# Optimization experiments

Measured on AMD Instinct MI355X. Metric: run time of the kernel, lower is better.

The kernel has to match this reference:

```python
import jax, jax.numpy as jnp
import numpy as np

NUM_EMBEDDINGS = 1024
EMBEDDING_DIM = 256
COMMITMENT_COST = 0.25


def setup_inputs() -> dict:
    key = jax.random.key(0)
    k1, k2 = jax.random.split(key)
    inputs = jax.random.normal(k1, (16, EMBEDDING_DIM, 4096), dtype=jnp.float32)
    # torch init: uniform(-1/K, 1/K)
    weight = jax.random.uniform(k2, (NUM_EMBEDDINGS, EMBEDDING_DIM), dtype=jnp.float32,
                                minval=-1.0 / NUM_EMBEDDINGS, maxval=1.0 / NUM_EMBEDDINGS)
    return {"inputs": inputs, "weight": weight}


def reference(inputs, weight):
    # [B, D, T] -> [B, T, D]
    x = jnp.transpose(inputs, (0, 2, 1))
    B, T, D = x.shape
    x_flat = x.reshape(-1, D)  # [N, D]
    distances = (jnp.sum(x_flat ** 2, axis=1, keepdims=True)
                 + jnp.sum(weight ** 2, axis=1)
                 - 2.0 * jnp.matmul(x_flat, weight.T))  # [N, K]
    encoding_indices = jnp.argmin(distances, axis=1)  # [N]
    # gather instead of one-hot matmul (same math)
    quantized = weight[encoding_indices].reshape(B, T, D)

    e_latent_loss = jnp.mean((jax.lax.stop_gradient(quantized) - x) ** 2)
    q_latent_loss = jnp.mean((quantized - jax.lax.stop_gradient(x)) ** 2)
    loss = q_latent_loss + COMMITMENT_COST * e_latent_loss

    # straight-through estimator
    quantized_st = x + jax.lax.stop_gradient(quantized - x)

    N = x_flat.shape[0]
    counts = jnp.zeros((weight.shape[0],), dtype=jnp.float32).at[encoding_indices].add(1.0)
    avg_probs = counts / N
    perplexity = jnp.exp(-jnp.sum(avg_probs * jnp.log(avg_probs + 1e-10)))

    return quantized_st, loss, perplexity, encoding_indices[:, None]
```

## Files before the change

### kernel.cpp

```cpp
#include <hip/hip_runtime.h>
#include <math.h>

#define B_ 16
#define D_ 256
#define T_ 4096
#define K_ 1024
#define N_ (B_*T_)

typedef __attribute__((ext_vector_type(8))) short short8;
typedef __attribute__((ext_vector_type(8))) unsigned short ushort8;
typedef __attribute__((ext_vector_type(4))) float f32x4;

#define CAND_MAX 24
#define EPS1 1.0e-3f
#define EPS2 5.0e-4f

__device__ __forceinline__ unsigned short f2bf(float f) {
  unsigned u = __float_as_uint(f);
  u += 0x7fffu + ((u >> 16) & 1u);
  return (unsigned short)(u >> 16);
}

__device__ __forceinline__ void gl_lds16(const void* g, void* l) {
  __builtin_amdgcn_global_load_lds((const __attribute__((address_space(1))) unsigned int*)g,
                                   (__attribute__((address_space(3))) unsigned int*)l,
                                   16, 0, 0);
}

__global__ void k_split(const float* __restrict__ x, unsigned short* __restrict__ xh) {
  __shared__ float xs[64 * 65];
  const int b = blockIdx.y, t0 = blockIdx.x * 64;
  const int tid = threadIdx.x;
  const int r = tid >> 4, cf = tid & 15;
  for (int dc = 0; dc < D_; dc += 64) {
#pragma unroll
    for (int p = 0; p < 4; ++p) {
      const int dd = r + p * 16;
      float4 v = *(const float4*)(x + (size_t)b * D_ * T_ + (size_t)(dc + dd) * T_ + t0 + cf * 4);
      xs[(cf * 4 + 0) * 65 + dd] = v.x;
      xs[(cf * 4 + 1) * 65 + dd] = v.y;
      xs[(cf * 4 + 2) * 65 + dd] = v.z;
      xs[(cf * 4 + 3) * 65 + dd] = v.w;
    }
    __syncthreads();
    const int c = tid & 7, row2 = tid >> 3;
#pragma unroll
    for (int p = 0; p < 2; ++p) {
      const int tt = row2 + p * 32;
      ushort8 hv;
#pragma unroll
      for (int j = 0; j < 8; ++j) hv[j] = f2bf(xs[tt * 65 + c * 8 + j]);
      *(ushort8*)(xh + (size_t)(b * T_ + t0 + tt) * D_ + dc + c * 8) = hv;
    }
    __syncthreads();
  }
}

__global__ void k_wsplit(const float* __restrict__ w, unsigned short* __restrict__ wh) {
  const int i = blockIdx.x * 256 + threadIdx.x;
  if (i < K_ * D_) wh[i] = f2bf(w[i]);
}

__global__ void k_wsq(const float* __restrict__ w, float* __restrict__ wsq) {
#pragma clang fp contract(off)
  const int k = blockIdx.x * 256 + threadIdx.x;
  const float* row = w + (size_t)k * D_;
  float h[2];
#pragma unroll
  for (int half = 0; half < 2; ++half) {
    const float* a = row + half * 128;
    float r[8];
#pragma unroll
    for (int j = 0; j < 8; ++j) { float v = a[j]; r[j] = v * v; }
    for (int i = 8; i < 128; i += 8) {
#pragma unroll
      for (int j = 0; j < 8; ++j) { float v = a[i + j]; r[j] += v * v; }
    }
    h[half] = ((r[0] + r[1]) + (r[2] + r[3])) + ((r[4] + r[5]) + (r[6] + r[7]));
  }
  wsq[k] = h[0] + h[1];
}

__global__ void k_xsq(const float* __restrict__ x, float* __restrict__ xsq) {
#pragma clang fp contract(off)
  const int t = blockIdx.x * 256 + threadIdx.x;
  const int b = blockIdx.y;
  const float* p = x + (size_t)b * D_ * T_ + t;
  float h[2];
#pragma unroll
  for (int half = 0; half < 2; ++half) {
    const float* ph = p + (size_t)half * 128 * T_;
    float r[8];
#pragma unroll
    for (int j = 0; j < 8; ++j) { float v = ph[(size_t)j * T_]; r[j] = v * v; }
    for (int i = 8; i < 128; i += 8) {
#pragma unroll
      for (int j = 0; j < 8; ++j) { float v = ph[(size_t)(i + j) * T_]; r[j] += v * v; }
    }
    h[half] = ((r[0] + r[1]) + (r[2] + r[3])) + ((r[4] + r[5]) + (r[6] + r[7]));
  }
  xsq[(size_t)b * T_ + t] = h[0] + h[1];
}

__launch_bounds__(256, 4)
__global__ void k_mfma(const unsigned short* __restrict__ xh, const unsigned short* __restrict__ wh,
                       const float* __restrict__ xsq, const float* __restrict__ wsq,
                       int* __restrict__ cnt, int2* __restrict__ cand) {
  __shared__ unsigned short Ah[128 * 32];
  __shared__ unsigned short Bh[128 * 32];
  const int tid = threadIdx.x;
  const int wave = tid >> 6, lane = tid & 63;
  const int col = lane & 15, quad = lane >> 4;
  const int n0 = blockIdx.x * 128;
  const int k0 = blockIdx.y * 128;
  const int wm = wave >> 1, wn = wave & 1;

  const int srow_base = (wave & 1) * 64;
  unsigned short* stile = (wave < 2) ? Ah : Bh;
  const unsigned short* sg = (wave < 2) ? (xh + (size_t)n0 * D_) : (wh + (size_t)k0 * D_);
  const int sq = (lane & 3) ^ ((lane >> 3) & 3);
  const int smrow = lane >> 2;

  int aoff[4], boff[4];
#pragma unroll
  for (int f = 0; f < 4; ++f) {
    const int mt = wm * 64 + f * 16 + col;
    aoff[f] = mt * 32 + (quad ^ ((col >> 1) & 3)) * 8;
    const int nt = wn * 64 + f * 16 + col;
    boff[f] = nt * 32 + (quad ^ ((col >> 1) & 3)) * 8;
  }

  f32x4 acc[4][4] = {};
  for (int dc = 0; dc < D_; dc += 32) {
#pragma unroll
    for (int i = 0; i < 4; ++i) {
      const int m = srow_base + i * 16 + smrow;
      gl_lds16(sg + (size_t)m * D_ + dc + sq * 8, &stile[(srow_base + i * 16) * 32]);
    }
    __syncthreads();
    short8 a[4], b[4];
#pragma unroll
    for (int f = 0; f < 4; ++f) a[f] = *(const short8*)(Ah + aoff[f]);
#pragma unroll
    for (int f = 0; f < 4; ++f) b[f] = *(const short8*)(Bh + boff[f]);
#pragma unroll
    for (int fm = 0; fm < 4; ++fm)
#pragma unroll
      for (int fn = 0; fn < 4; ++fn)
        acc[fm][fn] = __builtin_amdgcn_mfma_f32_16x16x32_bf16(a[fm], b[fn], acc[fm][fn], 0, 0, 0);
    __syncthreads();
  }

  float xq[4][4], wq[4];
#pragma unroll
  for (int fm = 0; fm < 4; ++fm)
#pragma unroll
    for (int r = 0; r < 4; ++r) xq[fm][r] = xsq[n0 + wm * 64 + fm * 16 + quad * 4 + r];
#pragma unroll
  for (int fn = 0; fn < 4; ++fn) wq[fn] = wsq[k0 + wn * 64 + fn * 16 + col];

  float rmin[4][4];
#pragma unroll
  for (int fm = 0; fm < 4; ++fm)
#pragma unroll
    for (int r = 0; r < 4; ++r) {
      float v = INFINITY;
#pragma unroll
      for (int fn = 0; fn < 4; ++fn) {
        const float s = (xq[fm][r] + wq[fn]) - 2.0f * acc[fm][fn][r];
        v = fminf(v, s);
      }
      v = fminf(v, __shfl_xor(v, 1));
      v = fminf(v, __shfl_xor(v, 2));
      v = fminf(v, __shfl_xor(v, 4));
      v = fminf(v, __shfl_xor(v, 8));
      rmin[fm][r] = v;
    }

  float* minbuf = (float*)Ah;
  if (col == 0) {
#pragma unroll
    for (int fm = 0; fm < 4; ++fm)
#pragma unroll
      for (int r = 0; r < 4; ++r)
        minbuf[(wm * 64 + fm * 16 + quad * 4 + r) * 2 + wn] = rmin[fm][r];
  }
  __syncthreads();

#pragma unroll
  for (int fm = 0; fm < 4; ++fm)
#pragma unroll
    for (int r = 0; r < 4; ++r) {
      const int m = wm * 64 + fm * 16 + quad * 4 + r;
      const float th = fminf(minbuf[2 * m], minbuf[2 * m + 1]) + EPS1;
#pragma unroll
      for (int fn = 0; fn < 4; ++fn) {
        const float s = (xq[fm][r] + wq[fn]) - 2.0f * acc[fm][fn][r];
        if (s <= th) {
          const int p = atomicAdd(&cnt[n0 + m], 1);
          if (p < CAND_MAX)
            cand[(size_t)(n0 + m) * CAND_MAX + p] =
                make_int2(k0 + wn * 64 + fn * 16 + col, __float_as_int(s));
        }
      }
    }
}

__global__ void k_rescore(const float* __restrict__ x, const float* __restrict__ w,
                          const float* __restrict__ xsq, const float* __restrict__ wsq,
                          const int* __restrict__ cnt, const int2* __restrict__ cand,
                          int* __restrict__ final_idx) {
  __shared__ float xrow[64 * 257];
  __shared__ unsigned int sbits[64];
  __shared__ unsigned long long fin[64];
  const int blk = blockIdx.x;
  const int b = (blk * 64) >> 12, t0 = (blk * 64) & (T_ - 1);
  const int tid = threadIdx.x;
  const int r = tid >> 4, cf = tid & 15;
  if (tid < 64) { sbits[tid] = 0xffffffffu; fin[tid] = ~0ULL; }
  for (int dc = 0; dc < D_; dc += 64) {
#pragma unroll
    for (int p = 0; p < 4; ++p) {
      const int dd = r + p * 16;
      float4 v = *(const float4*)(x + (size_t)b * D_ * T_ + (size_t)(dc + dd) * T_ + t0 + cf * 4);
      xrow[(cf * 4 + 0) * 257 + dc + dd] = v.x;
      xrow[(cf * 4 + 1) * 257 + dc + dd] = v.y;
      xrow[(cf * 4 + 2) * 257 + dc + dd] = v.z;
      xrow[(cf * 4 + 3) * 257 + dc + dd] = v.w;
    }
  }
  __syncthreads();
  const int row = tid & 63;
  const int n = blk * 64 + row;
  const int c0 = tid >> 6;
  const int nc = min(cnt[n], CAND_MAX);
  for (int c = c0; c < nc; c += 4)
    atomicMin(&sbits[row], (unsigned)cand[(size_t)n * CAND_MAX + c].y);
  __syncthreads();
  const float th = __uint_as_float(sbits[row]) + EPS2;
  const float xq = xsq[n];
  for (int c = c0; c < nc; c += 4) {
    const int2 e = cand[(size_t)n * CAND_MAX + c];
    if (__int_as_float(e.y) <= th) {
      const float* wr = w + (size_t)e.x * D_;
      float acc = 0.f;
#pragma unroll 8
      for (int d = 0; d < D_; ++d) acc = fmaf(xrow[row * 257 + d], wr[d], acc);
      const float s = (xq + wsq[e.x]) - 2.0f * acc;
      atomicMin(&fin[row], ((unsigned long long)__float_as_uint(s) << 32) | (unsigned)e.x);
    }
  }
  __syncthreads();
  if (tid < 64) final_idx[blk * 64 + tid] = (int)(fin[tid] & 0xffffffffULL);
}

__global__ void k_emit(const float* __restrict__ x, const float* __restrict__ w,
                       const int* __restrict__ fidx,
                       float* __restrict__ out0, float* __restrict__ out_idx,
                       int* __restrict__ counts, float* __restrict__ sumsq) {
  __shared__ float xs[64 * 65];
  __shared__ int sidx[64];
  __shared__ float sred[4];
  const int b = blockIdx.y, t0 = blockIdx.x * 64;
  const int tid = threadIdx.x;

  if (tid < 64) {
    const int n = b * T_ + t0 + tid;
    const int idx = fidx[n];
    sidx[tid] = idx;
    out_idx[n] = (float)idx;
    atomicAdd(&counts[idx], 1);
  }
  __syncthreads();

  const int r = tid >> 4;
  const int c = tid & 15;
  float lsum = 0.f;
  for (int dc = 0; dc < D_; dc += 64) {
#pragma unroll
    for (int p = 0; p < 4; ++p) {
      const int dd = r + p * 16;
      float4 v = *(const float4*)(x + (size_t)b * D_ * T_ + (size_t)(dc + dd) * T_ + t0 + c * 4);
      xs[(c * 4 + 0) * 65 + dd] = v.x;
      xs[(c * 4 + 1) * 65 + dd] = v.y;
      xs[(c * 4 + 2) * 65 + dd] = v.z;
      xs[(c * 4 + 3) * 65 + dd] = v.w;
    }
    __syncthreads();
    const int dx = tid & 15;
    const int tg = tid >> 4;
#pragma unroll
    for (int q = 0; q < 4; ++q) {
      const int t = q * 16 + tg;
      const int idx = sidx[t];
      const float4 wv = *(const float4*)(w + (size_t)idx * D_ + dc + dx * 4);
      const float x0 = xs[t * 65 + dx * 4 + 0];
      const float x1 = xs[t * 65 + dx * 4 + 1];
      const float x2 = xs[t * 65 + dx * 4 + 2];
      const float x3 = xs[t * 65 + dx * 4 + 3];
      const float d0 = wv.x - x0, d1 = wv.y - x1, d2 = wv.z - x2, d3 = wv.w - x3;
      float4 ov = make_float4(x0 + d0, x1 + d1, x2 + d2, x3 + d3);
      *(float4*)(out0 + (size_t)(b * T_ + t0 + t) * D_ + dc + dx * 4) = ov;
      lsum += d0 * d0 + d1 * d1 + d2 * d2 + d3 * d3;
    }
    __syncthreads();
  }
  for (int off = 32; off; off >>= 1) lsum += __shfl_down(lsum, off);
  if ((tid & 63) == 0) sred[tid >> 6] = lsum;
  __syncthreads();
  if (tid == 0) atomicAdd(sumsq, sred[0] + sred[1] + sred[2] + sred[3]);
}

__global__ void k_final(const int* __restrict__ counts, const float* __restrict__ sumsq,
                        float* __restrict__ out_scalars) {
  __shared__ float sred[4];
  const int tid = threadIdx.x;
  float s = 0.f;
  for (int k = tid; k < K_; k += 256) {
    const float p = (float)counts[k] / (float)N_;
    s += p * logf(p + 1e-10f);
  }
  for (int off = 32; off; off >>= 1) s += __shfl_down(s, off);
  if ((tid & 63) == 0) sred[tid >> 6] = s;
  __syncthreads();
  if (tid == 0) {
    const float ent = sred[0] + sred[1] + sred[2] + sred[3];
    const float m = sumsq[0] / 16777216.0f;
    out_scalars[0] = m + 0.25f * m;
    out_scalars[1] = expf(-ent);
  }
}

__global__ void k_wt(const float* __restrict__ w, float* __restrict__ wt) {
  __shared__ float tile[64][65];
  const int k0 = blockIdx.x * 64, d0 = blockIdx.y * 64;
  const int c = threadIdx.x & 15, r = threadIdx.x >> 4;
#pragma unroll
  for (int p = 0; p < 4; ++p) {
    const int kk = r + p * 16;
    float4 v = *(const float4*)(w + (size_t)(k0 + kk) * D_ + d0 + c * 4);
    tile[kk][c * 4 + 0] = v.x; tile[kk][c * 4 + 1] = v.y;
    tile[kk][c * 4 + 2] = v.z; tile[kk][c * 4 + 3] = v.w;
  }
  __syncthreads();
#pragma unroll
  for (int p = 0; p < 4; ++p) {
    const int dd = r + p * 16;
    float4 v = make_float4(tile[c * 4 + 0][dd], tile[c * 4 + 1][dd],
                           tile[c * 4 + 2][dd], tile[c * 4 + 3][dd]);
    *(float4*)(wt + (size_t)(d0 + dd) * K_ + k0 + c * 4) = v;
  }
}

__launch_bounds__(256, 4)
__global__ void k_argmin(const float* __restrict__ x, const float* __restrict__ wt,
                         const float* __restrict__ xsq, const float* __restrict__ wsq,
                         unsigned long long* __restrict__ packed) {
  extern __shared__ char smem[];
  float* Xs = (float*)smem;
  float* Ws = (float*)(smem + 32 * 128 * sizeof(float));
  const int tid = threadIdx.x;
  const int tx = tid & 15, ty = tid >> 4;
  const int n0 = blockIdx.x * 128, k0 = blockIdx.y * 128;
  const int b = n0 >> 12, t0 = n0 & (T_ - 1);
  const float* xbase = x + (size_t)b * D_ * T_ + t0;
  const float* wbase = wt + k0;
  float acc[8][8];
#pragma unroll
  for (int i = 0; i < 8; ++i)
#pragma unroll
    for (int j = 0; j < 8; ++j) acc[i][j] = 0.f;
  const int sr = tid >> 5, sc = tid & 31;
  for (int dc = 0; dc < D_; dc += 32) {
#pragma unroll
    for (int p = 0; p < 4; ++p) {
      const int rr = sr + p * 8;
      const float4 xv = *(const float4*)(xbase + (size_t)(dc + rr) * T_ + sc * 4);
      *(float4*)(Xs + rr * 128 + sc * 4) = xv;
      const float4 wv = *(const float4*)(wbase + (size_t)(dc + rr) * K_ + sc * 4);
      *(float4*)(Ws + rr * 128 + sc * 4) = wv;
    }
    __syncthreads();
#pragma unroll 4
    for (int d = 0; d < 32; ++d) {
      const float4 xa = *(const float4*)(Xs + d * 128 + tx * 8);
      const float4 xb = *(const float4*)(Xs + d * 128 + tx * 8 + 4);
      const float4 wa = *(const float4*)(Ws + d * 128 + ty * 8);
      const float4 wb = *(const float4*)(Ws + d * 128 + ty * 8 + 4);
      const float xr[8] = {xa.x, xa.y, xa.z, xa.w, xb.x, xb.y, xb.z, xb.w};
      const float wr[8] = {wa.x, wa.y, wa.z, wa.w, wb.x, wb.y, wb.z, wb.w};
#pragma unroll
      for (int i = 0; i < 8; ++i)
#pragma unroll
        for (int j = 0; j < 8; ++j)
          acc[i][j] = fmaf(xr[i], wr[j], acc[i][j]);
    }
    __syncthreads();
  }
  float xq[8];
#pragma unroll
  for (int i = 0; i < 8; ++i) xq[i] = xsq[n0 + tx * 8 + i];
  float best[8]; int bidx[8];
#pragma unroll
  for (int i = 0; i < 8; ++i) { best[i] = INFINITY; bidx[i] = 0; }
#pragma unroll
  for (int j = 0; j < 8; ++j) {
    const int kk = k0 + ty * 8 + j;
    const float wq = wsq[kk];
#pragma unroll
    for (int i = 0; i < 8; ++i) {
      const float s = (xq[i] + wq) - 2.0f * acc[i][j];
      if (s < best[i]) { best[i] = s; bidx[i] = kk; }
    }
  }
  float* rv = (float*)smem;
  int* ri = (int*)(smem + 16 * 128 * sizeof(float));
#pragma unroll
  for (int i = 0; i < 8; ++i) {
    rv[ty * 128 + tx * 8 + i] = best[i];
    ri[ty * 128 + tx * 8 + i] = bidx[i];
  }
  __syncthreads();
  if (tid < 128) {
    float bv = rv[tid]; int bi = ri[tid];
#pragma unroll
    for (int u = 1; u < 16; ++u) {
      const float v = rv[u * 128 + tid];
      const int ii = ri[u * 128 + tid];
      if (v < bv || (v == bv && ii < bi)) { bv = v; bi = ii; }
    }
    const unsigned long long pk =
        ((unsigned long long)__float_as_uint(bv) << 32) | (unsigned int)bi;
    atomicMin(packed + n0 + tid, pk);
  }
}

__global__ void k_unpack(const unsigned long long* __restrict__ p, int* __restrict__ fi) {
  const int i = blockIdx.x * 256 + threadIdx.x;
  fi[i] = (int)(p[i] & 0xffffffffULL);
}

extern "C" void kernel_launch(void* const* d_in, const int* in_sizes, int n_in,
                              void* d_out, int out_size, void* d_ws, size_t ws_size,
                              hipStream_t stream) {
  const float* x = (const float*)d_in[0];
  const float* w = (const float*)d_in[1];
  float* out = (float*)d_out;
  float* out0 = out;
  float* out_scalars = out + 16777216;
  float* out_idx = out + 16777218;

  char* ws = (char*)d_ws;
  const size_t NEED = 48u * 1024u * 1024u;

  if (ws_size >= NEED) {
    unsigned short* xh = (unsigned short*)ws;
    unsigned short* wh = (unsigned short*)(ws + 33554432);
    float* xsq = (float*)(ws + 34078720);
    float* wsq = (float*)(ws + 34340864);
    int* cnt = (int*)(ws + 34344960);
    int2* cand = (int2*)(ws + 34607104);
    int* final_idx = (int*)(ws + 47190016);
    int* counts = (int*)(ws + 47452160);
    float* sumsq = (float*)(ws + 47456256);

    hipMemsetAsync(cnt, 0, 262144, stream);
    hipMemsetAsync(counts, 0, 4096 + 256, stream);

    k_split<<<dim3(T_ / 64, B_), dim3(256), 0, stream>>>(x, xh);
    k_wsplit<<<dim3((K_ * D_) / 256), dim3(256), 0, stream>>>(w, wh);
    k_wsq<<<dim3(K_ / 256), dim3(256), 0, stream>>>(w, wsq);
    k_xsq<<<dim3(T_ / 256, B_), dim3(256), 0, stream>>>(x, xsq);
    k_mfma<<<dim3(N_ / 128, K_ / 128), dim3(256), 0, stream>>>(xh, wh, xsq, wsq, cnt, cand);
    k_rescore<<<dim3(N_ / 64), dim3(256), 0, stream>>>(x, w, xsq, wsq, cnt, cand, final_idx);
    k_emit<<<dim3(T_ / 64, B_), dim3(256), 0, stream>>>(x, w, final_idx, out0, out_idx, counts, sumsq);
    k_final<<<1, 256, 0, stream>>>(counts, sumsq, out_scalars);
  } else {
    unsigned long long* packed = (unsigned long long*)ws;
    int* counts = (int*)(ws + 524288);
    float* sumsq = (float*)(ws + 528384);
    float* wsq = (float*)(ws + 528640);
    float* xsq = (float*)(ws + 532736);
    float* wt = (float*)(ws + 794880);
    int* final_idx = (int*)(ws + 1843200);

    hipMemsetAsync(packed, 0xFF, 524288, stream);
    hipMemsetAsync(counts, 0, 4096 + 256, stream);

    k_wt<<<dim3(K_ / 64, D_ / 64), dim3(256), 0, stream>>>(w, wt);
    k_wsq<<<dim3(K_ / 256), dim3(256), 0, stream>>>(w, wsq);
    k_xsq<<<dim3(T_ / 256, B_), dim3(256), 0, stream>>>(x, xsq);
    k_argmin<<<dim3(N_ / 128, K_ / 128), dim3(256), 32 * 1024, stream>>>(x, wt, xsq, wsq, packed);
    k_unpack<<<dim3(N_ / 256), dim3(256), 0, stream>>>(packed, final_idx);
    k_emit<<<dim3(T_ / 64, B_), dim3(256), 0, stream>>>(x, w, final_idx, out0, out_idx, counts, sumsq);
    k_final<<<1, 256, 0, stream>>>(counts, sumsq, out_scalars);
  }
}
```

Baseline: 383.0 us.

## Keep token tile in registers and stream codebook through double-buffered LDS

The MFMA distance kernel changes from a 2D grid of 128x128 tiles to one block per 256 tokens. Each wave holds its 64 tokens' bf16 rows in registers and sweeps the full codebook in 64-entry chunks, double-buffered in LDS. A running per-token minimum replaces the cross-wave shared-memory minimum exchange and the re-reads of x tiles across K blocks. The cost is heavy register pressure (launch bounds drop to one block) and a looser threshold early in the sweep, which may push more candidates through the atomics.

```diff
diff --git a/kernel.cpp b/kernel.cpp
--- a/kernel.cpp
+++ b/kernel.cpp
@@ -102,108 +102,107 @@
   xsq[(size_t)b * T_ + t] = h[0] + h[1];
 }
 
-__launch_bounds__(256, 4)
+__launch_bounds__(256, 1)
 __global__ void k_mfma(const unsigned short* __restrict__ xh, const unsigned short* __restrict__ wh,
                        const float* __restrict__ xsq, const float* __restrict__ wsq,
                        int* __restrict__ cnt, int2* __restrict__ cand) {
-  __shared__ unsigned short Ah[128 * 32];
-  __shared__ unsigned short Bh[128 * 32];
+  __shared__ unsigned short Wl[2][16384];
   const int tid = threadIdx.x;
   const int wave = tid >> 6, lane = tid & 63;
   const int col = lane & 15, quad = lane >> 4;
-  const int n0 = blockIdx.x * 128;
-  const int k0 = blockIdx.y * 128;
-  const int wm = wave >> 1, wn = wave & 1;
-
-  const int srow_base = (wave & 1) * 64;
-  unsigned short* stile = (wave < 2) ? Ah : Bh;
-  const unsigned short* sg = (wave < 2) ? (xh + (size_t)n0 * D_) : (wh + (size_t)k0 * D_);
-  const int sq = (lane & 3) ^ ((lane >> 3) & 3);
-  const int smrow = lane >> 2;
-
-  int aoff[4], boff[4];
-#pragma unroll
-  for (int f = 0; f < 4; ++f) {
-    const int mt = wm * 64 + f * 16 + col;
-    aoff[f] = mt * 32 + (quad ^ ((col >> 1) & 3)) * 8;
-    const int nt = wn * 64 + f * 16 + col;
-    boff[f] = nt * 32 + (quad ^ ((col >> 1) & 3)) * 8;
-  }
-
-  f32x4 acc[4][4] = {};
-  for (int dc = 0; dc < D_; dc += 32) {
-#pragma unroll
-    for (int i = 0; i < 4; ++i) {
-      const int m = srow_base + i * 16 + smrow;
-      gl_lds16(sg + (size_t)m * D_ + dc + sq * 8, &stile[(srow_base + i * 16) * 32]);
-    }
-    __syncthreads();
-    short8 a[4], b[4];
-#pragma unroll
-    for (int f = 0; f < 4; ++f) a[f] = *(const short8*)(Ah + aoff[f]);
-#pragma unroll
-    for (int f = 0; f < 4; ++f) b[f] = *(const short8*)(Bh + boff[f]);
+  const int n0 = blockIdx.x * 256;
+  const int tok0 = n0 + wave * 64;
+
+  short8 A[8][4];
+#pragma unroll
+  for (int dg = 0; dg < 8; ++dg)
 #pragma unroll
     for (int fm = 0; fm < 4; ++fm)
+      A[dg][fm] = *(const short8*)(xh + (size_t)(tok0 + fm * 16 + col) * D_ + dg * 32 + quad * 8);
+
+  float xq[4][4];
+#pragma unroll
+  for (int fm = 0; fm < 4; ++fm)
+#pragma unroll
+    for (int r = 0; r < 4; ++r)
+      xq[fm][r] = xsq[tok0 + fm * 16 + quad * 4 + r];
+
+  float runmin[4][4];
+#pragma unroll
+  for (int fm = 0; fm < 4; ++fm)
+#pragma unroll
+    for (int r = 0; r < 4; ++r) runmin[fm][r] = INFINITY;
+
+  const int srow = lane >> 2;
+  const int gq = (lane & 3) ^ ((lane >> 3) & 3);
+
+#define STAGE(KC, HALF)                                                          \
+  {                                                                              \
+    const unsigned short* wsrc =                                                 \
+        wh + (size_t)((KC) * 64 + wave * 16 + srow) * D_ + gq * 8;               \
+    unsigned short* dstb = &Wl[HALF][wave * 512];                                \
+    _Pragma("unroll")                                                            \
+    for (int dg = 0; dg < 8; ++dg)                                               \
+      gl_lds16(wsrc + dg * 32, dstb + dg * 2048);                                \
+  }
+
+  STAGE(0, 0)
+  __syncthreads();
+
+  for (int kc = 0; kc < 16; ++kc) {
+    const int half = kc & 1;
+    if (kc < 15) STAGE(kc + 1, half ^ 1)
+
+    f32x4 acc[4][4] = {};
+    const unsigned short* Wb = Wl[half];
+#pragma unroll
+    for (int dg = 0; dg < 8; ++dg) {
+      short8 b[4];
 #pragma unroll
       for (int fn = 0; fn < 4; ++fn)
-        acc[fm][fn] = __builtin_amdgcn_mfma_f32_16x16x32_bf16(a[fm], b[fn], acc[fm][fn], 0, 0, 0);
-    __syncthreads();
-  }
-
-  float xq[4][4], wq[4];
-#pragma unroll
-  for (int fm = 0; fm < 4; ++fm)
-#pragma unroll
-    for (int r = 0; r < 4; ++r) xq[fm][r] = xsq[n0 + wm * 64 + fm * 16 + quad * 4 + r];
-#pragma unroll
-  for (int fn = 0; fn < 4; ++fn) wq[fn] = wsq[k0 + wn * 64 + fn * 16 + col];
-
-  float rmin[4][4];
-#pragma unroll
-  for (int fm = 0; fm < 4; ++fm)
-#pragma unroll
-    for (int r = 0; r < 4; ++r) {
-      float v = INFINITY;
-#pragma unroll
-      for (int fn = 0; fn < 4; ++fn) {
-        const float s = (xq[fm][r] + wq[fn]) - 2.0f * acc[fm][fn][r];
-        v = fminf(v, s);
-      }
-      v = fminf(v, __shfl_xor(v, 1));
-      v = fminf(v, __shfl_xor(v, 2));
-      v = fminf(v, __shfl_xor(v, 4));
-      v = fminf(v, __shfl_xor(v, 8));
-      rmin[fm][r] = v;
-    }
-
-  float* minbuf = (float*)Ah;
-  if (col == 0) {
+        b[fn] = *(const short8*)(Wb + dg * 2048 + (fn * 16 + col) * 32 +
+                                 (quad ^ ((col >> 1) & 3)) * 8);
+#pragma unroll
+      for (int fm = 0; fm < 4; ++fm)
+#pragma unroll
+        for (int fn = 0; fn < 4; ++fn)
+          acc[fm][fn] = __builtin_amdgcn_mfma_f32_16x16x32_bf16(A[dg][fm], b[fn], acc[fm][fn], 0, 0, 0);
+    }
+
+    float wq[4];
+#pragma unroll
+    for (int fn = 0; fn < 4; ++fn) wq[fn] = wsq[kc * 64 + fn * 16 + col];
+
 #pragma unroll
     for (int fm = 0; fm < 4; ++fm)
 #pragma unroll
-      for (int r = 0; r < 4; ++r)
-        minbuf[(wm * 64 + fm * 16 + quad * 4 + r) * 2 + wn] = rmin[fm][r];
-  }
-  __syncthreads();
-
-#pragma unroll
-  for (int fm = 0; fm < 4; ++fm)
-#pragma unroll
-    for (int r = 0; r < 4; ++r) {
-      const int m = wm * 64 + fm * 16 + quad * 4 + r;
-      const float th = fminf(minbuf[2 * m], minbuf[2 * m + 1]) + EPS1;
-#pragma unroll
-      for (int fn = 0; fn < 4; ++fn) {
-        const float s = (xq[fm][r] + wq[fn]) - 2.0f * acc[fm][fn][r];
-        if (s <= th) {
-          const int p = atomicAdd(&cnt[n0 + m], 1);
-          if (p < CAND_MAX)
-            cand[(size_t)(n0 + m) * CAND_MAX + p] =
-                make_int2(k0 + wn * 64 + fn * 16 + col, __float_as_int(s));
+      for (int r = 0; r < 4; ++r) {
+        float s[4];
+        float v = INFINITY;
+#pragma unroll
+        for (int fn = 0; fn < 4; ++fn) {
+          s[fn] = (xq[fm][r] + wq[fn]) - 2.0f * acc[fm][fn][r];
+          v = fminf(v, s[fn]);
+        }
+        v = fminf(v, __shfl_xor(v, 1));
+        v = fminf(v, __shfl_xor(v, 2));
+        v = fminf(v, __shfl_xor(v, 4));
+        v = fminf(v, __shfl_xor(v, 8));
+        runmin[fm][r] = fminf(runmin[fm][r], v);
+        const float thr = runmin[fm][r] + EPS1;
+        const int n = tok0 + fm * 16 + quad * 4 + r;
+#pragma unroll
+        for (int fn = 0; fn < 4; ++fn) {
+          if (s[fn] <= thr) {
+            const int p = atomicAdd(&cnt[n], 1);
+            if (p < CAND_MAX)
+              cand[(size_t)n * CAND_MAX + p] =
+                  make_int2(kc * 64 + fn * 16 + col, __float_as_int(s[fn]));
+          }
         }
       }
-    }
+    __syncthreads();
+  }
 }
 
 __global__ void k_rescore(const float* __restrict__ x, const float* __restrict__ w,
@@ -471,7 +470,7 @@
     k_wsplit<<<dim3((K_ * D_) / 256), dim3(256), 0, stream>>>(w, wh);
     k_wsq<<<dim3(K_ / 256), dim3(256), 0, stream>>>(w, wsq);
     k_xsq<<<dim3(T_ / 256, B_), dim3(256), 0, stream>>>(x, xsq);
-    k_mfma<<<dim3(N_ / 128, K_ / 128), dim3(256), 0, stream>>>(xh, wh, xsq, wsq, cnt, cand);
+    k_mfma<<<dim3(N_ / 256), dim3(256), 0, stream>>>(xh, wh, xsq, wsq, cnt, cand);
     k_rescore<<<dim3(N_ / 64), dim3(256), 0, stream>>>(x, w, xsq, wsq, cnt, cand, final_idx);
     k_emit<<<dim3(T_ / 64, B_), dim3(256), 0, stream>>>(x, w, final_idx, out0, out_idx, counts, sumsq);
     k_final<<<1, 256, 0, stream>>>(counts, sumsq, out_scalars);
```

Result: slower. 423.8 us (+10.7%).
